# Kernel tuning notes

Hardware: AMD Instinct MI355X
Metric: run time of the kernel (lower is better)

Reference implementation:

```python
import jax, jax.numpy as jnp
import numpy as np


def setup_inputs() -> dict:
    key = jax.random.key(0)
    ks = jax.random.split(key, 12)
    B, L, N, C, Ct, H, RH1, RH2, S = 64, 64, 256, 8, 4, 128, 128, 64, 4
    def rn(k, shape, s=0.08):
        return jax.random.normal(k, shape, dtype=jnp.float32) * s
    return dict(
        x=jax.random.normal(ks[0], (B, L, N, C * Ct), dtype=jnp.float32),
        hidden_intensity=jax.random.normal(ks[1], (B, N, H), dtype=jnp.float32),
        r=jax.random.normal(ks[2], (B, S), dtype=jnp.float32),
        W_ih=rn(ks[3], (4 * H, C)), W_hh=rn(ks[4], (4 * H, H)),
        b_ih=jnp.zeros((4 * H,), jnp.float32), b_hh=jnp.zeros((4 * H,), jnp.float32),
        W1=rn(ks[5], (RH1, 2 * H + 1)), b1=jnp.zeros((RH1,), jnp.float32),
        W2=rn(ks[6], (RH2, RH1)), b2=jnp.zeros((RH2,), jnp.float32),
        W3=rn(ks[7], (C, RH2)), b3=jnp.zeros((C,), jnp.float32),
        Wf=rn(ks[8], (1, C)), bf=jnp.zeros((1,), jnp.float32),
    )


def reference(x, hidden_intensity, r, W_ih, W_hh, b_ih, b_hh,
              W1, b1, W2, b2, W3, b3, Wf, bf):
    # Faithful to torch: nn.LSTM has batch_first=False but is fed (B, L, C),
    # so B is the sequence axis, L the batch axis, and lstm_out[:, -1, :]
    # writes predictions into that last column, so only x[:, -1] matters.
    B, L, N, _ = x.shape
    C = W_ih.shape[1]
    Ct = x.shape[3] // C
    H = W_hh.shape[1]

    def lstm_all_times(seq):  # seq: (T, Bb, C) -> hidden at every time (T, Bb, H)
        xp = jnp.einsum('tbc,gc->tbg', seq, W_ih) + b_ih + b_hh  # (T, Bb, 4H)
        def step(carry, xt):
            h, c = carry
            g = xt + h @ W_hh.T
            i, f, gg, o = jnp.split(g, 4, axis=-1)  # torch gate order i,f,g,o
            c = jax.nn.sigmoid(f) * c + jax.nn.sigmoid(i) * jnp.tanh(gg)
            h = jax.nn.sigmoid(o) * jnp.tanh(c)
            return (h, c), h
        z0 = jnp.zeros((seq.shape[1], H), seq.dtype)
        _, hs = jax.lax.scan(step, (z0, z0), xp)
        return hs

    hi = jnp.broadcast_to(hidden_intensity[:, :, None, :], (B, N, Ct, H))

    def roll(last_col, rj):  # last_col: (B, N, Ct, C), rj: (B,)
        hs = lstm_all_times(last_col.reshape(B, N * Ct, C)).reshape(B, N, Ct, H)
        rr = jnp.broadcast_to(rj[:, None, None, None], (B, N, Ct, 1))
        z = jnp.concatenate([hs, hi, rr], axis=-1)       # (B, N, Ct, 2H+1)
        h1 = jax.nn.relu(z @ W1.T + b1)
        h2 = jax.nn.relu(h1 @ W2.T + b2)
        pr = h2 @ W3.T + b3                              # (B, N, Ct, C)
        contrib = (jax.nn.relu(pr) @ Wf.T + bf)[..., 0].sum(axis=2)  # (B, N)
        return pr, contrib

    last0 = x[:, -1, :, :].reshape(B, N, Ct, C)
    _, preds = jax.lax.scan(roll, last0, r.T)  # (S, B, N)
    return jnp.transpose(preds, (1, 2, 0))     # (B, N, steps_ahead)
```

## Files before the change

kernel.cpp:

```cpp
#include <hip/hip_runtime.h>
#include <hip/hip_bf16.h>


typedef __attribute__((ext_vector_type(8))) _Float16 half8;
typedef __attribute__((ext_vector_type(4))) float f32x4;

#define MFMAH(a, b, c) __builtin_amdgcn_mfma_f32_16x16x32_f16(a, b, c, 0, 0, 0)

__device__ __forceinline__ float sigf(float x)   { return 1.0f / (1.0f + __expf(-x)); }
__device__ __forceinline__ float tanh_f(float x) { return 1.0f - 2.0f / (__expf(2.0f * x) + 1.0f); }

__global__ void init_cur_k(const float* __restrict__ x, _Float16* __restrict__ cur16)
{
    int i   = blockIdx.x * 256 + threadIdx.x;
    int b   = i >> 13;
    int rem = i & 8191;
    cur16[i] = (_Float16)x[(size_t)b * 524288 + 63 * 8192 + rem];
}

__global__ void cvt_hi_k(const float* __restrict__ hi, _Float16* __restrict__ hi16)
{
    int i = blockIdx.x * 256 + threadIdx.x;
    hi16[i] = (_Float16)hi[i];
}

__global__ void pack_w_k(const float* __restrict__ W1, const float* __restrict__ W2,
                         const float* __restrict__ W3, _Float16* __restrict__ wp1,
                         _Float16* __restrict__ wp2, _Float16* __restrict__ wp3)
{
    int i = blockIdx.x * 256 + threadIdx.x;
    if (i < 32768) {
        int fragid = i >> 9, lj = i & 511;
        int kt = fragid >> 3, nt = fragid & 7;
        int l = lj >> 3, j = lj & 7;
        int k = kt * 32 + (l >> 4) * 8 + j;
        int o = nt * 16 + (l & 15);
        wp1[i] = (_Float16)W1[o * 257 + k];
    } else if (i < 32768 + 8192) {
        int ii = i - 32768;
        int fragid = ii >> 9, lj = ii & 511;
        int kt = fragid >> 2, nt = fragid & 3;
        int l = lj >> 3, j = lj & 7;
        int k = kt * 32 + (l >> 4) * 8 + j;
        int o = nt * 16 + (l & 15);
        wp2[ii] = (_Float16)W2[o * 128 + k];
    } else if (i < 32768 + 8192 + 1024) {
        int ii = i - 32768 - 8192;
        int kt = ii >> 9, lj = ii & 511;
        int l = lj >> 3, j = lj & 7;
        int k = kt * 32 + (l >> 4) * 8 + j;
        int c = l & 15;
        wp3[ii] = (_Float16)((c < 8) ? W3[c * 64 + k] : 0.0f);
    }
}

__global__ void pack_wB_k(const float* __restrict__ W_hh, const float* __restrict__ W_ih,
                          _Float16* __restrict__ wpB)
{
    int i = blockIdx.x * 256 + threadIdx.x;
    if (i >= 81920) return;
    int frag = i >> 9, lj = i & 511;
    int kt = frag >> 5, ntile = frag & 31;
    int l = lj >> 3, j = lj & 7;
    int klocal = (l >> 4) * 8 + j;
    int col = ntile * 16 + (l & 15);
    float v;
    if (kt < 4)      v = W_hh[col * 128 + kt * 32 + klocal];
    else             v = (klocal < 8) ? W_ih[col * 8 + klocal] : 0.0f;
    wpB[i] = (_Float16)v;
}

__global__ __launch_bounds__(512, 2) void lstm_mfma_k(
    const _Float16* __restrict__ cur16, const _Float16* __restrict__ wpB,
    const float* __restrict__ b_ih, const float* __restrict__ b_hh,
    _Float16* __restrict__ hs16)
{
    __shared__ __align__(16) _Float16 zone[2][4][640];
    __shared__ __align__(16) _Float16 xz[64][32];

    const int t  = threadIdx.x;
    const int cg = t >> 6, l = t & 63;
    const int li = l & 15, lk = l >> 4;
    const int q0 = blockIdx.x * 4;

    half8 bw[4][5];
#pragma unroll
    for (int g = 0; g < 4; ++g)
#pragma unroll
        for (int kt = 0; kt < 5; ++kt) {
            bw[g][kt] = *(const half8*)(wpB + (size_t)(kt * 32 + g * 8 + cg) * 512 + l * 8);
            asm volatile("" : "+a"(bw[g][kt]));
        }

    float bsum[4];
#pragma unroll
    for (int g = 0; g < 4; ++g) {
        int gc = g * 128 + cg * 16 + li;
        bsum[g] = b_ih[gc] + b_hh[gc];
    }

    for (int i = t; i < 2560; i += 512) ((uint*)zone)[i] = 0;
    if (t < 256) {
        int step = t >> 2, tt = t & 3;
        *(uint4*)&xz[step][tt * 8] =
            *(const uint4*)(cur16 + (size_t)step * 8192 + q0 * 8 + tt * 8);
    }
    float cc = 0.0f;
    __syncthreads();

    const int zpl   = cg >> 1;
    const int jl    = (cg & 1) * 16 + li;
    const int roff  = (li & 12) * 40 + lk * 8;
    const int srow  = lk * 4;

    _Float16* ph = hs16 + (size_t)(q0 + lk) * 128 + cg * 16 + li;
    const _Float16* xrd = &xz[0][(li >> 2) * 8];

    auto dostep = [&](int step, int p) {
        const int pn = p ^ 1;
        half8 xa = *(const half8*)(xrd + step * 32);

        half8 ah[4];
#pragma unroll
        for (int kt = 0; kt < 4; ++kt)
            ah[kt] = *(const half8*)&zone[p][kt][roff];

        f32x4 acc[4];
#pragma unroll
        for (int g = 0; g < 4; ++g)
            acc[g] = (f32x4){bsum[g], bsum[g], bsum[g], bsum[g]};
#pragma unroll
        for (int kt = 0; kt < 4; ++kt)
#pragma unroll
            for (int g = 0; g < 4; ++g)
                acc[g] = MFMAH(ah[kt], bw[g][kt], acc[g]);
#pragma unroll
        for (int g = 0; g < 4; ++g)
            acc[g] = MFMAH(xa, bw[g][4], acc[g]);

        float pi = acc[0][0], pf = acc[1][0], pg = acc[2][0], po = acc[3][0];
        cc = sigf(pf) * cc + sigf(pi) * tanh_f(pg);
        float hv = sigf(po) * tanh_f(cc);
        _Float16 h16 = (_Float16)hv;
        zone[pn][zpl][srow * 40 + jl] = h16;
        ph[(size_t)step * 131072] = h16;
        asm volatile("s_waitcnt lgkmcnt(0)\n\ts_barrier" ::: "memory");
    };

    for (int s2 = 0; s2 < 32; ++s2) {
        dostep(s2 * 2,     0);
        dostep(s2 * 2 + 1, 1);
    }
}

__global__ __launch_bounds__(256, 2) void mlp_mfma_k(
    const _Float16* __restrict__ hs16, const _Float16* __restrict__ hi16,
    const float* __restrict__ r, int jstep,
    const _Float16* __restrict__ wp1, const _Float16* __restrict__ wp2,
    const _Float16* __restrict__ wp3,
    const float* __restrict__ W1, const float* __restrict__ b1,
    const float* __restrict__ b2, const float* __restrict__ b3,
    const float* __restrict__ Wf, const float* __restrict__ bfp,
    _Float16* __restrict__ cur16, float* __restrict__ out)
{
    __shared__ __align__(16) _Float16 h1f[4 * 4 * 640];
    __shared__ __align__(16) _Float16 h2f[2 * 4 * 640];

    const int t = threadIdx.x;
    const int w = t >> 6, l = t & 63;
    const int lrow = l & 15, lk = l >> 4;
    const int b = blockIdx.x >> 4;
    const int qb = (blockIdx.x & 15) * 64;
    const float rb = r[b * 4 + jstep];

    f32x4 acc[4][2];
#pragma unroll
    for (int nt = 0; nt < 2; ++nt) {
        int col = w * 32 + nt * 16 + lrow;
        float bias = b1[col] + rb * W1[col * 257 + 256];
#pragma unroll
        for (int mt = 0; mt < 4; ++mt)
            acc[mt][nt] = (f32x4){bias, bias, bias, bias};
    }

#pragma unroll 4
    for (int kt = 0; kt < 8; ++kt) {
        half8 av[4];
#pragma unroll
        for (int mt = 0; mt < 4; ++mt) {
            int q = qb + mt * 16 + lrow;
            if (kt < 4) {
                av[mt] = *(const half8*)(hs16 + (size_t)(b * 1024 + q) * 128
                                          + kt * 32 + lk * 8);
            } else {
                av[mt] = *(const half8*)(hi16 + (size_t)(b * 256 + (q >> 2)) * 128
                                          + (kt - 4) * 32 + lk * 8);
            }
        }
#pragma unroll
        for (int nt = 0; nt < 2; ++nt) {
            half8 bv = *(const half8*)(wp1 + (size_t)(kt * 8 + w * 2 + nt) * 512 + l * 8);
#pragma unroll
            for (int mt = 0; mt < 4; ++mt)
                acc[mt][nt] = MFMAH(av[mt], bv, acc[mt][nt]);
        }
    }

#pragma unroll
    for (int mt = 0; mt < 4; ++mt)
#pragma unroll
        for (int nt = 0; nt < 2; ++nt)
#pragma unroll
            for (int reg = 0; reg < 4; ++reg) {
                float v = fmaxf(acc[mt][nt][reg], 0.0f);
                int s = lk * 4 + reg, jj = nt * 16 + lrow;
                h1f[(w * 4 + mt) * 640 + s * 40 + jj] = (_Float16)v;
            }
    __syncthreads();

    f32x4 acc2[4];
    {
        float bias = b2[16 * w + lrow];
#pragma unroll
        for (int mt = 0; mt < 4; ++mt)
            acc2[mt] = (f32x4){bias, bias, bias, bias};
    }
#pragma unroll
    for (int kt = 0; kt < 4; ++kt) {
        half8 bv = *(const half8*)(wp2 + (size_t)(kt * 4 + w) * 512 + l * 8);
#pragma unroll
        for (int mt = 0; mt < 4; ++mt) {
            half8 a = *(const half8*)&h1f[(kt * 4 + mt) * 640 + lrow * 40 + lk * 8];
            acc2[mt] = MFMAH(a, bv, acc2[mt]);
        }
    }
#pragma unroll
    for (int mt = 0; mt < 4; ++mt)
#pragma unroll
        for (int reg = 0; reg < 4; ++reg) {
            float v = fmaxf(acc2[mt][reg], 0.0f);
            int s = lk * 4 + reg, jl2 = (w & 1) * 16 + lrow;
            h2f[((w >> 1) * 4 + mt) * 640 + s * 40 + jl2] = (_Float16)v;
        }
    __syncthreads();

    f32x4 acc3 = (f32x4){0.0f, 0.0f, 0.0f, 0.0f};
#pragma unroll
    for (int kt = 0; kt < 2; ++kt) {
        half8 a  = *(const half8*)&h2f[(kt * 4 + w) * 640 + lrow * 40 + lk * 8];
        half8 bv = *(const half8*)(wp3 + (size_t)kt * 512 + l * 8);
        acc3 = MFMAH(a, bv, acc3);
    }

    const int c = lrow;
    const float b3v = (c < 8) ? b3[c] : 0.0f;
    const float wfv = (c < 8) ? Wf[c] : 0.0f;
    float fr[4];
#pragma unroll
    for (int reg = 0; reg < 4; ++reg) {
        float pr = acc3[reg] + b3v;
        if (c < 8) {
            int row = 16 * w + lk * 4 + reg;
            cur16[((size_t)(b * 1024 + qb + row)) * 8 + c] = (_Float16)pr;
        }
        fr[reg] = (c < 8) ? fmaxf(pr, 0.0f) * wfv : 0.0f;
    }
#pragma unroll
    for (int reg = 0; reg < 4; ++reg) {
        fr[reg] += __shfl_xor(fr[reg], 1);
        fr[reg] += __shfl_xor(fr[reg], 2);
        fr[reg] += __shfl_xor(fr[reg], 4);
    }
    if ((l & 15) == 0) {
        int n = (qb + 16 * w + lk * 4) >> 2;
        float v = fr[0] + fr[1] + fr[2] + fr[3] + 4.0f * bfp[0];
        out[(size_t)(b * 256 + n) * 4 + jstep] = v;
    }
}

extern "C" void kernel_launch(void* const* d_in, const int* in_sizes, int n_in,
                              void* d_out, int out_size, void* d_ws, size_t ws_size,
                              hipStream_t stream)
{
    const float* x   = (const float*)d_in[0];
    const float* hi  = (const float*)d_in[1];
    const float* r   = (const float*)d_in[2];
    const float* Wih = (const float*)d_in[3];
    const float* Whh = (const float*)d_in[4];
    const float* bih = (const float*)d_in[5];
    const float* bhh = (const float*)d_in[6];
    const float* W1  = (const float*)d_in[7];
    const float* b1  = (const float*)d_in[8];
    const float* W2  = (const float*)d_in[9];
    const float* b2  = (const float*)d_in[10];
    const float* W3  = (const float*)d_in[11];
    const float* b3  = (const float*)d_in[12];
    const float* Wf  = (const float*)d_in[13];
    const float* bf  = (const float*)d_in[14];
    float* out = (float*)d_out;

    _Float16* cur16 = (_Float16*)d_ws;
    _Float16* hs16  = cur16 + 524288;
    _Float16* hi16  = hs16 + 8388608;
    _Float16* wp1   = hi16 + 2097152;
    _Float16* wp2   = wp1 + 32768;
    _Float16* wp3   = wp2 + 8192;
    _Float16* wpB   = wp3 + 1024;

    init_cur_k<<<2048, 256, 0, stream>>>(x, cur16);
    cvt_hi_k<<<8192, 256, 0, stream>>>(hi, hi16);
    pack_w_k<<<164, 256, 0, stream>>>(W1, W2, W3, wp1, wp2, wp3);
    pack_wB_k<<<320, 256, 0, stream>>>(Whh, Wih, wpB);
    for (int j = 0; j < 4; ++j) {
        lstm_mfma_k<<<256, 512, 0, stream>>>(cur16, wpB, bih, bhh, hs16);
        mlp_mfma_k<<<1024, 256, 0, stream>>>(hs16, hi16, r, j, wp1, wp2, wp3,
                                             W1, b1, b2, b3, Wf, bf, cur16, out);
    }
}
```

Before: 283.4 us.

## Merge prep kernels, hoist input-projection MFMA off the LSTM critical path

Four preprocessing launches (input slice convert, hidden-intensity convert, MLP weight pack, LSTM weight pack) become one kernel, removing launch gaps. In the LSTM recurrence, the input-projection MFMA for the next step is issued after the barrier so it runs off the dependent h-chain, and the recurrent MFMAs are split into two independent accumulator chains, which shortens the serial dependency per step. The zone zero-init loop is narrowed and the MLP kernel's launch bounds are raised to 3 blocks per CU, which may increase register pressure or spilling.

```diff
diff --git a/kernel.cpp b/kernel.cpp
--- a/kernel.cpp
+++ b/kernel.cpp
@@ -10,25 +10,23 @@
 __device__ __forceinline__ float sigf(float x)   { return 1.0f / (1.0f + __expf(-x)); }
 __device__ __forceinline__ float tanh_f(float x) { return 1.0f - 2.0f / (__expf(2.0f * x) + 1.0f); }
 
-__global__ void init_cur_k(const float* __restrict__ x, _Float16* __restrict__ cur16)
-{
-    int i   = blockIdx.x * 256 + threadIdx.x;
-    int b   = i >> 13;
-    int rem = i & 8191;
-    cur16[i] = (_Float16)x[(size_t)b * 524288 + 63 * 8192 + rem];
-}
-
-__global__ void cvt_hi_k(const float* __restrict__ hi, _Float16* __restrict__ hi16)
+__global__ void prep_k(const float* __restrict__ x, const float* __restrict__ hi,
+                       const float* __restrict__ W1, const float* __restrict__ W2,
+                       const float* __restrict__ W3, const float* __restrict__ W_hh,
+                       const float* __restrict__ W_ih,
+                       _Float16* __restrict__ cur16, _Float16* __restrict__ hi16,
+                       _Float16* __restrict__ wp1, _Float16* __restrict__ wp2,
+                       _Float16* __restrict__ wp3, _Float16* __restrict__ wpB)
 {
     int i = blockIdx.x * 256 + threadIdx.x;
-    hi16[i] = (_Float16)hi[i];
-}
-
-__global__ void pack_w_k(const float* __restrict__ W1, const float* __restrict__ W2,
-                         const float* __restrict__ W3, _Float16* __restrict__ wp1,
-                         _Float16* __restrict__ wp2, _Float16* __restrict__ wp3)
-{
-    int i = blockIdx.x * 256 + threadIdx.x;
+    if (i < 524288) {
+        int b = i >> 13, rem = i & 8191;
+        cur16[i] = (_Float16)x[(size_t)b * 524288 + 63 * 8192 + rem];
+        return;
+    }
+    i -= 524288;
+    if (i < 2097152) { hi16[i] = (_Float16)hi[i]; return; }
+    i -= 2097152;
     if (i < 32768) {
         int fragid = i >> 9, lj = i & 511;
         int kt = fragid >> 3, nt = fragid & 7;
@@ -36,38 +34,39 @@
         int k = kt * 32 + (l >> 4) * 8 + j;
         int o = nt * 16 + (l & 15);
         wp1[i] = (_Float16)W1[o * 257 + k];
-    } else if (i < 32768 + 8192) {
-        int ii = i - 32768;
-        int fragid = ii >> 9, lj = ii & 511;
+        return;
+    }
+    i -= 32768;
+    if (i < 8192) {
+        int fragid = i >> 9, lj = i & 511;
         int kt = fragid >> 2, nt = fragid & 3;
         int l = lj >> 3, j = lj & 7;
         int k = kt * 32 + (l >> 4) * 8 + j;
         int o = nt * 16 + (l & 15);
-        wp2[ii] = (_Float16)W2[o * 128 + k];
-    } else if (i < 32768 + 8192 + 1024) {
-        int ii = i - 32768 - 8192;
-        int kt = ii >> 9, lj = ii & 511;
+        wp2[i] = (_Float16)W2[o * 128 + k];
+        return;
+    }
+    i -= 8192;
+    if (i < 1024) {
+        int kt = i >> 9, lj = i & 511;
         int l = lj >> 3, j = lj & 7;
         int k = kt * 32 + (l >> 4) * 8 + j;
         int c = l & 15;
-        wp3[ii] = (_Float16)((c < 8) ? W3[c * 64 + k] : 0.0f);
-    }
-}
-
-__global__ void pack_wB_k(const float* __restrict__ W_hh, const float* __restrict__ W_ih,
-                          _Float16* __restrict__ wpB)
-{
-    int i = blockIdx.x * 256 + threadIdx.x;
-    if (i >= 81920) return;
-    int frag = i >> 9, lj = i & 511;
-    int kt = frag >> 5, ntile = frag & 31;
-    int l = lj >> 3, j = lj & 7;
-    int klocal = (l >> 4) * 8 + j;
-    int col = ntile * 16 + (l & 15);
-    float v;
-    if (kt < 4)      v = W_hh[col * 128 + kt * 32 + klocal];
-    else             v = (klocal < 8) ? W_ih[col * 8 + klocal] : 0.0f;
-    wpB[i] = (_Float16)v;
+        wp3[i] = (_Float16)((c < 8) ? W3[c * 64 + k] : 0.0f);
+        return;
+    }
+    i -= 1024;
+    if (i < 81920) {
+        int frag = i >> 9, lj = i & 511;
+        int kt = frag >> 5, ntile = frag & 31;
+        int l = lj >> 3, j = lj & 7;
+        int klocal = (l >> 4) * 8 + j;
+        int col = ntile * 16 + (l & 15);
+        float v;
+        if (kt < 4) v = W_hh[col * 128 + kt * 32 + klocal];
+        else        v = (klocal < 8) ? W_ih[col * 8 + klocal] : 0.0f;
+        wpB[i] = (_Float16)v;
+    }
 }
 
 __global__ __launch_bounds__(512, 2) void lstm_mfma_k(
@@ -92,14 +91,15 @@
             asm volatile("" : "+a"(bw[g][kt]));
         }
 
-    float bsum[4];
+    f32x4 bs4[4];
 #pragma unroll
     for (int g = 0; g < 4; ++g) {
         int gc = g * 128 + cg * 16 + li;
-        bsum[g] = b_ih[gc] + b_hh[gc];
-    }
-
-    for (int i = t; i < 2560; i += 512) ((uint*)zone)[i] = 0;
+        float bv = b_ih[gc] + b_hh[gc];
+        bs4[g] = (f32x4){bv, bv, bv, bv};
+    }
+
+    for (int i = t; i < 1280; i += 512) ((uint*)zone)[i] = 0;
     if (t < 256) {
         int step = t >> 2, tt = t & 3;
         *(uint4*)&xz[step][tt * 8] =
@@ -116,35 +116,50 @@
     _Float16* ph = hs16 + (size_t)(q0 + lk) * 128 + cg * 16 + li;
     const _Float16* xrd = &xz[0][(li >> 2) * 8];
 
+    f32x4 accx[4];
+    {
+        half8 xa0 = *(const half8*)(xrd);
+#pragma unroll
+        for (int g = 0; g < 4; ++g)
+            accx[g] = MFMAH(xa0, bw[g][4], bs4[g]);
+    }
+
     auto dostep = [&](int step, int p) {
         const int pn = p ^ 1;
-        half8 xa = *(const half8*)(xrd + step * 32);
 
         half8 ah[4];
 #pragma unroll
         for (int kt = 0; kt < 4; ++kt)
             ah[kt] = *(const half8*)&zone[p][kt][roff];
 
-        f32x4 acc[4];
-#pragma unroll
-        for (int g = 0; g < 4; ++g)
-            acc[g] = (f32x4){bsum[g], bsum[g], bsum[g], bsum[g]};
-#pragma unroll
-        for (int kt = 0; kt < 4; ++kt)
-#pragma unroll
-            for (int g = 0; g < 4; ++g)
-                acc[g] = MFMAH(ah[kt], bw[g][kt], acc[g]);
-#pragma unroll
-        for (int g = 0; g < 4; ++g)
-            acc[g] = MFMAH(xa, bw[g][4], acc[g]);
-
-        float pi = acc[0][0], pf = acc[1][0], pg = acc[2][0], po = acc[3][0];
+        const f32x4 z4 = (f32x4){0.0f, 0.0f, 0.0f, 0.0f};
+        f32x4 a0[4], a1[4];
+#pragma unroll
+        for (int g = 0; g < 4; ++g) {
+            a0[g] = MFMAH(ah[0], bw[g][0], accx[g]);
+            a1[g] = MFMAH(ah[2], bw[g][2], z4);
+        }
+#pragma unroll
+        for (int g = 0; g < 4; ++g) {
+            a0[g] = MFMAH(ah[1], bw[g][1], a0[g]);
+            a1[g] = MFMAH(ah[3], bw[g][3], a1[g]);
+        }
+
+        float pi = a0[0][0] + a1[0][0];
+        float pf = a0[1][0] + a1[1][0];
+        float pg = a0[2][0] + a1[2][0];
+        float po = a0[3][0] + a1[3][0];
         cc = sigf(pf) * cc + sigf(pi) * tanh_f(pg);
         float hv = sigf(po) * tanh_f(cc);
         _Float16 h16 = (_Float16)hv;
         zone[pn][zpl][srow * 40 + jl] = h16;
         ph[(size_t)step * 131072] = h16;
         asm volatile("s_waitcnt lgkmcnt(0)\n\ts_barrier" ::: "memory");
+
+        half8 xn = *(const half8*)(xrd + ((step + 1) & 63) * 32);
+#pragma unroll
+        for (int g = 0; g < 4; ++g)
+            accx[g] = MFMAH(xn, bw[g][4], bs4[g]);
     };
 
     for (int s2 = 0; s2 < 32; ++s2) {
@@ -153,7 +168,7 @@
     }
 }
 
-__global__ __launch_bounds__(256, 2) void mlp_mfma_k(
+__global__ __launch_bounds__(256, 3) void mlp_mfma_k(
     const _Float16* __restrict__ hs16, const _Float16* __restrict__ hi16,
     const float* __restrict__ r, int jstep,
     const _Float16* __restrict__ wp1, const _Float16* __restrict__ wp2,
@@ -307,10 +322,8 @@
     _Float16* wp3   = wp2 + 8192;
     _Float16* wpB   = wp3 + 1024;
 
-    init_cur_k<<<2048, 256, 0, stream>>>(x, cur16);
-    cvt_hi_k<<<8192, 256, 0, stream>>>(hi, hi16);
-    pack_w_k<<<164, 256, 0, stream>>>(W1, W2, W3, wp1, wp2, wp3);
-    pack_wB_k<<<320, 256, 0, stream>>>(Whh, Wih, wpB);
+    prep_k<<<10724, 256, 0, stream>>>(x, hi, W1, W2, W3, Whh, Wih,
+                                      cur16, hi16, wp1, wp2, wp3, wpB);
     for (int j = 0; j < 4; ++j) {
         lstm_mfma_k<<<256, 512, 0, stream>>>(cur16, wpB, bih, bhh, hs16);
         mlp_mfma_k<<<1024, 256, 0, stream>>>(hs16, hi16, r, j, wp1, wp2, wp3,
```

Result: no change. 286.7 us (+1.2%).
